# Kernel optimization log

Hardware: AMD Instinct MI355X
Metric: run time of the kernel (lower is better)

## Reference

```python
import jax, jax.numpy as jnp
import numpy as np

N = 50000      # nodes per node type
E = 600000     # edges per edge type
H = 128        # hidden_channels (= in_channels)
OUT = 16       # out_channels
G = 64         # number of graphs in the batch
L = 2          # num_layers
NEG_SLOPE = 0.2


def setup_inputs() -> dict:
    key = jax.random.key(0)
    ks = jax.random.split(key, 13)
    x_paper = jax.random.normal(ks[0], (N, H), jnp.float32)
    x_author = jax.random.normal(ks[1], (N, H), jnp.float32)
    edge_pa = jax.random.randint(ks[2], (2, E), 0, N, jnp.int32)   # paper -> author
    edge_ap = jax.random.randint(ks[3], (2, E), 0, N, jnp.int32)   # author -> paper
    batch_paper = jnp.sort(jax.random.randint(ks[4], (N,), 0, G, jnp.int32))
    batch_author = jnp.sort(jax.random.randint(ks[5], (N,), 0, G, jnp.int32))
    # GAT params, stacked [layer, edge_type, ...]; edge_type 0 = paper->author, 1 = author->paper
    Wsrc = jax.random.normal(ks[6], (L, 2, H, H), jnp.float32) * 0.05
    Wdst = jax.random.normal(ks[7], (L, 2, H, H), jnp.float32) * 0.05
    att_src = jax.random.normal(ks[8], (L, 2, H), jnp.float32) * 0.05
    att_dst = jax.random.normal(ks[9], (L, 2, H), jnp.float32) * 0.05
    bias = jax.random.normal(ks[10], (L, 2, H), jnp.float32) * 0.05
    linW = jax.random.normal(ks[11], (H, OUT), jnp.float32) * 0.05
    linb = jax.random.normal(ks[12], (OUT,), jnp.float32) * 0.05
    return {"x_paper": x_paper, "x_author": x_author, "edge_pa": edge_pa,
            "edge_ap": edge_ap, "batch_paper": batch_paper, "batch_author": batch_author,
            "Wsrc": Wsrc, "Wdst": Wdst, "att_src": att_src, "att_dst": att_dst,
            "bias": bias, "linW": linW, "linb": linb}


def _gat(x_s, x_d, edge, Wsrc, Wdst, a_src_w, a_dst_w, b):
    """Single-head PyG GATConv (bipartite, add_self_loops=False, concat)."""
    src, dst = edge[0], edge[1]
    hs = x_s @ Wsrc                        # [Ns, H]
    hd = x_d @ Wdst                        # [Nd, H]
    a_s = hs @ a_src_w                     # [Ns]
    a_d = hd @ a_dst_w                     # [Nd]
    e = jax.nn.leaky_relu(a_s[src] + a_d[dst], NEG_SLOPE)   # [E]
    nd = x_d.shape[0]
    m = jax.ops.segment_max(e, dst, num_segments=nd)        # segment softmax
    ex = jnp.exp(e - m[dst])
    den = jax.ops.segment_sum(ex, dst, num_segments=nd) + 1e-16
    w = ex / den[dst]                                        # [E]
    out = jax.ops.segment_sum(w[:, None] * hs[src], dst, num_segments=nd)
    return out + b


def reference(x_paper, x_author, edge_pa, edge_ap, batch_paper, batch_author,
              Wsrc, Wdst, att_src, att_dst, bias, linW, linb):
    xp, xa = x_paper, x_author
    for l in range(L):
        out_a = _gat(xp, xa, edge_pa, Wsrc[l, 0], Wdst[l, 0], att_src[l, 0], att_dst[l, 0], bias[l, 0])
        out_p = _gat(xa, xp, edge_ap, Wsrc[l, 1], Wdst[l, 1], att_src[l, 1], att_dst[l, 1], bias[l, 1])
        xp = jax.nn.relu(out_p)
        xa = jax.nn.relu(out_a)
    pooled_p = jax.ops.segment_max(xp, batch_paper, num_segments=G)  # [G, H]
    pooled_a = jax.ops.segment_max(xa, batch_author, num_segments=G)
    return (pooled_p @ linW + linb, pooled_a @ linW + linb)
```

## Files before the change

kernel.cpp:

```cpp
#include <hip/hip_runtime.h>
#include <hip/hip_fp16.h>

constexpr int NN = 50000;
constexpr int NE = 600000;
constexpr int HH = 128;
constexpr int GG = 64;
constexpr int LL = 2;
constexpr int OC = 16;
constexpr float NEG = 0.2f;
constexpr int NBK = (2 * NN + 255) / 256;

typedef _Float16 f16x8 __attribute__((ext_vector_type(8)));
typedef float f32x4 __attribute__((ext_vector_type(4)));

__global__ void k_prevec(const float* __restrict__ Wsrc, const float* __restrict__ Wdst,
                         const float* __restrict__ att_src, const float* __restrict__ att_dst,
                         float* __restrict__ v) {
    int b = blockIdx.x;
    int kind = b >> 2, lt = b & 3;
    const float* W   = (kind ? Wdst : Wsrc) + (size_t)lt * HH * HH;
    const float* att = (kind ? att_dst : att_src) + lt * HH;
    __shared__ float sa[HH];
    int t = threadIdx.x;
    sa[t] = att[t];
    __syncthreads();
    float s = 0.f;
    for (int j = 0; j < HH; ++j) s += W[t * HH + j] * sa[j];
    v[b * HH + t] = s;
}

__global__ void k_wcvt(const float* __restrict__ Wsrc, __half* __restrict__ Wt) {
    int lt = blockIdx.x >> 7;
    int nrow = blockIdx.x & 127;
    int k = threadIdx.x;
    Wt[((size_t)lt * HH + nrow) * HH + k] =
        __float2half_rn(Wsrc[(size_t)lt * HH * HH + (size_t)k * HH + nrow]);
}

__global__ void k_hist2(const int* __restrict__ dpa, const int* __restrict__ dap,
                        int* __restrict__ cnt) {
    int i = blockIdx.x * 256 + threadIdx.x;
    if (i < NE) atomicAdd(&cnt[dpa[i]], 1);
    else if (i < 2 * NE) atomicAdd(&cnt[NN + dap[i - NE]], 1);
}

__global__ void k_scan1(const int* __restrict__ cnt, int* __restrict__ bsum, int n) {
    __shared__ int s[256];
    int i = blockIdx.x * 256 + threadIdx.x;
    s[threadIdx.x] = (i < n) ? cnt[i] : 0;
    __syncthreads();
    for (int off = 128; off > 0; off >>= 1) {
        if (threadIdx.x < off) s[threadIdx.x] += s[threadIdx.x + off];
        __syncthreads();
    }
    if (threadIdx.x == 0) bsum[blockIdx.x] = s[0];
}

__global__ void k_scan2(int* __restrict__ bsum, int nb) {
    __shared__ int s[512];
    int t = threadIdx.x;
    int v = (t < nb) ? bsum[t] : 0;
    s[t] = v;
    __syncthreads();
    for (int off = 1; off < 512; off <<= 1) {
        int x = (t >= off) ? s[t - off] : 0;
        __syncthreads();
        s[t] += x;
        __syncthreads();
    }
    if (t < nb) bsum[t] = s[t] - v;
}

__global__ void k_scan3(const int* __restrict__ cnt, const int* __restrict__ bsum,
                        int* __restrict__ rowptr, int n, int e) {
    __shared__ int s[256];
    int t = threadIdx.x;
    int i = blockIdx.x * 256 + t;
    int v = (i < n) ? cnt[i] : 0;
    s[t] = v;
    __syncthreads();
    for (int off = 1; off < 256; off <<= 1) {
        int x = (t >= off) ? s[t - off] : 0;
        __syncthreads();
        s[t] += x;
        __syncthreads();
    }
    if (i < n) rowptr[i] = bsum[blockIdx.x] + s[t] - v;
    if (i == n - 1) rowptr[n] = e;
}

__global__ void k_binit(const int* __restrict__ rpc, int* __restrict__ bcur) {
    int b = blockIdx.x * 256 + threadIdx.x;
    if (b < NBK) bcur[b] = rpc[b * 256];
}

__global__ __launch_bounds__(256) void k_bucket1(const int* __restrict__ edge_pa,
                                                 const int* __restrict__ edge_ap,
                                                 int* __restrict__ bcur, unsigned* __restrict__ colt) {
    __shared__ int cnt[NBK];
    __shared__ int gpos[NBK];
    int t = threadIdx.x;
    int e0 = blockIdx.x * 4096;
    int m = min(4096, 2 * NE - e0);
    for (int i = t; i < NBK; i += 256) cnt[i] = 0;
    __syncthreads();
    for (int i = t; i < m; i += 256) {
        int e = e0 + i;
        int d = (e < NE) ? edge_pa[NE + e] : NN + edge_ap[NE + (e - NE)];
        atomicAdd(&cnt[d >> 8], 1);
    }
    __syncthreads();
    for (int b = t; b < NBK; b += 256)
        if (cnt[b]) gpos[b] = atomicAdd(&bcur[b], cnt[b]);
    __syncthreads();
    for (int i = t; i < m; i += 256) {
        int e = e0 + i;
        int src, d;
        if (e < NE) { src = edge_pa[e]; d = edge_pa[NE + e]; }
        else        { int j = e - NE; src = edge_ap[j]; d = NN + edge_ap[NE + j]; }
        int p = atomicAdd(&gpos[d >> 8], 1);
        colt[p] = ((unsigned)src << 8) | (unsigned)(d & 255);
    }
}

__global__ __launch_bounds__(256) void k_bucket2(const unsigned* __restrict__ colt,
                                                 const int* __restrict__ rpc,
                                                 int* __restrict__ colc, int* __restrict__ dstc) {
    __shared__ int cur[257];
    int b = blockIdx.x, t = threadIdx.x;
    int node0 = b * 256;
    int nn2 = min(256, 2 * NN - node0);
    for (int i = t; i <= nn2; i += 256) cur[i] = rpc[node0 + i];
    __syncthreads();
    int g0 = cur[0], g1 = cur[nn2];
    __syncthreads();
    for (int i = g0 + t; i < g1; i += 256) {
        unsigned p = colt[i];
        int pos = atomicAdd(&cur[p & 255], 1);
        colc[pos] = (int)(p >> 8);
        dstc[pos] = node0 + (int)(p & 255);
    }
}

__global__ __launch_bounds__(256) void k_gemm(const float* __restrict__ X, const __half* __restrict__ Wt,
                                              const float* __restrict__ v1, const float* __restrict__ v2,
                                              __half* __restrict__ Hout,
                                              float* __restrict__ o1, float* __restrict__ o2, int n) {
    int wave = threadIdx.x >> 6;
    int lane = threadIdx.x & 63;
    int r0 = blockIdx.x * 64 + wave * 16;
    int arow = r0 + (lane & 15);
    int kgrp = (lane >> 4) * 8;

    f32x4 acc[8] = {};
    float s1 = 0.f, s2 = 0.f;
#pragma unroll
    for (int ks = 0; ks < 4; ++ks) {
        int k0 = ks * 32 + kgrp;
        float xv[8];
        if (arow < n) {
            float4 x0 = *(const float4*)(X + (size_t)arow * HH + k0);
            float4 x1 = *(const float4*)(X + (size_t)arow * HH + k0 + 4);
            xv[0] = x0.x; xv[1] = x0.y; xv[2] = x0.z; xv[3] = x0.w;
            xv[4] = x1.x; xv[5] = x1.y; xv[6] = x1.z; xv[7] = x1.w;
        } else {
#pragma unroll
            for (int i = 0; i < 8; ++i) xv[i] = 0.f;
        }
        float4 va0 = *(const float4*)(v1 + k0), va1 = *(const float4*)(v1 + k0 + 4);
        float4 vb0 = *(const float4*)(v2 + k0), vb1 = *(const float4*)(v2 + k0 + 4);
        s1 += xv[0] * va0.x + xv[1] * va0.y + xv[2] * va0.z + xv[3] * va0.w
            + xv[4] * va1.x + xv[5] * va1.y + xv[6] * va1.z + xv[7] * va1.w;
        s2 += xv[0] * vb0.x + xv[1] * vb0.y + xv[2] * vb0.z + xv[3] * vb0.w
            + xv[4] * vb1.x + xv[5] * vb1.y + xv[6] * vb1.z + xv[7] * vb1.w;

        f16x8 ahi, alo;
#pragma unroll
        for (int i = 0; i < 8; ++i) {
            _Float16 h = (_Float16)xv[i];
            ahi[i] = h;
            alo[i] = (_Float16)(xv[i] - (float)h);
        }
#pragma unroll
        for (int nt = 0; nt < 8; ++nt) {
            const f16x8 b = *(const f16x8*)(Wt + ((size_t)(nt * 16 + (lane & 15))) * HH + k0);
            acc[nt] = __builtin_amdgcn_mfma_f32_16x16x32_f16(alo, b, acc[nt], 0, 0, 0);
            acc[nt] = __builtin_amdgcn_mfma_f32_16x16x32_f16(ahi, b, acc[nt], 0, 0, 0);
        }
    }

    s1 += __shfl_xor(s1, 16); s1 += __shfl_xor(s1, 32);
    s2 += __shfl_xor(s2, 16); s2 += __shfl_xor(s2, 32);
    if ((lane >> 4) == 0 && arow < n) { o1[arow] = s1; o2[arow] = s2; }

    int srow = r0 + (lane >> 4) * 4;
    int scol = lane & 15;
#pragma unroll
    for (int nt = 0; nt < 8; ++nt) {
#pragma unroll
        for (int reg = 0; reg < 4; ++reg) {
            int gr = srow + reg;
            if (gr < n) Hout[(size_t)gr * HH + nt * 16 + scol] = __float2half_rn(acc[nt][reg]);
        }
    }
}

__global__ __launch_bounds__(256) void k_score(const int* __restrict__ colc, const int* __restrict__ dstc,
                                               const float* __restrict__ as0, const float* __restrict__ as1,
                                               const float* __restrict__ adc, float* __restrict__ expw) {
    int j = blockIdx.x * 256 + threadIdx.x;
    if (j >= 2 * NE) return;
    int src = colc[j];
    int d   = dstc[j];
    float c = (j < NE ? as0 : as1)[src] + adc[d];
    c = c > 0.f ? c : NEG * c;
    expw[j] = __expf(c);
}

__global__ __launch_bounds__(256) void k_aggregate3(const int* __restrict__ rpc, const int* __restrict__ colc,
                                                    const float* __restrict__ expw,
                                                    const __half* __restrict__ H0, const __half* __restrict__ H1,
                                                    const float* __restrict__ bias0, const float* __restrict__ bias1,
                                                    float* __restrict__ XA, float* __restrict__ XP) {
    int wid  = (blockIdx.x * blockDim.x + threadIdx.x) >> 6;
    int lane = threadIdx.x & 63;
    int half = lane >> 5;
    int sl   = lane & 31;
    int w = wid * 2 + half;
    if (w >= 2 * NN) return;
    int type = (w >= NN);
    int node = type ? w - NN : w;
    const __half* Hs  = type ? H1 : H0;
    const float* bias = type ? bias1 : bias0;
    float* Xout       = type ? XP : XA;

    int base = rpc[w], end = rpc[w + 1];

    float den = 0.f;
    float4 acc = {0.f, 0.f, 0.f, 0.f};

    int j = base;
    for (; j + 4 <= end; j += 4) {
        int s[4]; float wg[4]; float2 raw[4];
#pragma unroll
        for (int k = 0; k < 4; ++k) s[k] = colc[j + k];
#pragma unroll
        for (int k = 0; k < 4; ++k) wg[k] = expw[j + k];
#pragma unroll
        for (int k = 0; k < 4; ++k) raw[k] = *(const float2*)(Hs + (size_t)s[k] * HH + sl * 4);
#pragma unroll
        for (int k = 0; k < 4; ++k) {
            den += wg[k];
            float2 fa = __half22float2(*(const __half2*)&raw[k].x);
            float2 fb = __half22float2(*(const __half2*)&raw[k].y);
            acc.x += wg[k] * fa.x; acc.y += wg[k] * fa.y;
            acc.z += wg[k] * fb.x; acc.w += wg[k] * fb.y;
        }
    }
    for (; j < end; ++j) {
        int s = colc[j];
        float wg = expw[j];
        float2 raw = *(const float2*)(Hs + (size_t)s * HH + sl * 4);
        den += wg;
        float2 fa = __half22float2(*(const __half2*)&raw.x);
        float2 fb = __half22float2(*(const __half2*)&raw.y);
        acc.x += wg * fa.x; acc.y += wg * fa.y;
        acc.z += wg * fb.x; acc.w += wg * fb.y;
    }

    float inv = 1.f / (den + 1e-16f);
    float4 b = *(const float4*)(bias + sl * 4);
    float4 o;
    o.x = fmaxf(acc.x * inv + b.x, 0.f);
    o.y = fmaxf(acc.y * inv + b.y, 0.f);
    o.z = fmaxf(acc.z * inv + b.z, 0.f);
    o.w = fmaxf(acc.w * inv + b.w, 0.f);
    *(float4*)(Xout + (size_t)node * HH + sl * 4) = o;
}

constexpr int POOL_CHUNK = 64;
__global__ __launch_bounds__(256) void k_pool(const float* __restrict__ XPf, const float* __restrict__ XAf,
                                              const int* __restrict__ batch_p, const int* __restrict__ batch_a,
                                              unsigned* __restrict__ pooled, int n, int blocksPerType) {
    int type = blockIdx.x / blocksPerType;
    int blk  = blockIdx.x % blocksPerType;
    const float* X = type ? XAf : XPf;
    const int* batch = type ? batch_a : batch_p;
    unsigned* pool = pooled + type * GG * HH;

    int sub  = threadIdx.x >> 5;
    int lane = threadIdx.x & 31;
    int i0 = blk * POOL_CHUNK + sub * (POOL_CHUNK / 8);
    if (i0 >= n) return;
    int i1 = min(i0 + POOL_CHUNK / 8, n);

    int g = batch[i0];
    float4 m = make_float4(0.f, 0.f, 0.f, 0.f);
    for (int i = i0; i < i1; ++i) {
        int gi = batch[i];
        if (gi != g) {
            unsigned* p = pool + g * HH + lane * 4;
            atomicMax(p + 0, __float_as_uint(m.x));
            atomicMax(p + 1, __float_as_uint(m.y));
            atomicMax(p + 2, __float_as_uint(m.z));
            atomicMax(p + 3, __float_as_uint(m.w));
            m = make_float4(0.f, 0.f, 0.f, 0.f);
            g = gi;
        }
        float4 x = *(const float4*)(X + (size_t)i * HH + lane * 4);
        m.x = fmaxf(m.x, x.x);
        m.y = fmaxf(m.y, x.y);
        m.z = fmaxf(m.z, x.z);
        m.w = fmaxf(m.w, x.w);
    }
    unsigned* p = pool + g * HH + lane * 4;
    atomicMax(p + 0, __float_as_uint(m.x));
    atomicMax(p + 1, __float_as_uint(m.y));
    atomicMax(p + 2, __float_as_uint(m.z));
    atomicMax(p + 3, __float_as_uint(m.w));
}

__global__ void k_final(const unsigned* __restrict__ pooled, const float* __restrict__ linW,
                        const float* __restrict__ linb, float* __restrict__ out) {
    int idx = blockIdx.x * blockDim.x + threadIdx.x;
    if (idx >= 2 * GG * OC) return;
    int p = idx >> 10;
    int g = (idx >> 4) & 63;
    int o = idx & 15;
    const unsigned* row = pooled + (size_t)(p * GG + g) * HH;
    float s = linb[o];
    for (int k = 0; k < HH; ++k) s += __uint_as_float(row[k]) * linW[k * OC + o];
    out[idx] = s;
}

extern "C" void kernel_launch(void* const* d_in, const int* in_sizes, int n_in,
                              void* d_out, int out_size, void* d_ws, size_t ws_size,
                              hipStream_t stream) {
    const float* x_paper  = (const float*)d_in[0];
    const float* x_author = (const float*)d_in[1];
    const int*   edge_pa  = (const int*)d_in[2];
    const int*   edge_ap  = (const int*)d_in[3];
    const int*   batch_p  = (const int*)d_in[4];
    const int*   batch_a  = (const int*)d_in[5];
    const float* Wsrc     = (const float*)d_in[6];
    const float* Wdst     = (const float*)d_in[7];
    const float* att_src  = (const float*)d_in[8];
    const float* att_dst  = (const float*)d_in[9];
    const float* bias     = (const float*)d_in[10];
    const float* linW     = (const float*)d_in[11];
    const float* linb     = (const float*)d_in[12];
    float* out = (float*)d_out;

    size_t off = 0;
    char* base = (char*)d_ws;
    auto alloc = [&](size_t bytes) -> void* {
        void* p = base + off;
        off += (bytes + 255) & ~(size_t)255;
        return p;
    };
    __half* H0 = (__half*)alloc((size_t)NN * HH * 2);
    __half* H1 = (__half*)alloc((size_t)NN * HH * 2);
    float* XP  = (float*)alloc((size_t)NN * HH * 4);
    float* XA  = (float*)alloc((size_t)NN * HH * 4);
    float* as0 = (float*)alloc(NN * 4);
    float* as1 = (float*)alloc(NN * 4);
    float* adc = (float*)alloc(2 * NN * 4);
    float* vv  = (float*)alloc(8 * HH * 4);
    __half* Wt = (__half*)alloc(4 * HH * HH * 2);
    int* rpc  = (int*)alloc((2 * NN + 1) * 4);
    int* colc = (int*)alloc(2 * NE * 4);
    int* dstc = (int*)alloc(2 * NE * 4);
    unsigned* colt = (unsigned*)alloc(2 * NE * 4);
    float* expw = (float*)alloc(2 * NE * 4);
    int* cnt  = (int*)alloc(2 * NN * 4);
    int* bsum = (int*)alloc(2048);
    int* bcur = (int*)alloc(NBK * 4);
    unsigned* pooled = (unsigned*)alloc(2 * GG * HH * 4);

    const int EB2  = (2 * NE + 255) / 256;
    const int NBS2 = (2 * NN + 255) / 256;
    const int CB   = (2 * NE + 4095) / 4096;

    k_prevec<<<8, 128, 0, stream>>>(Wsrc, Wdst, att_src, att_dst, vv);
    k_wcvt<<<512, 128, 0, stream>>>(Wsrc, Wt);

    hipMemsetAsync(cnt, 0, 2 * NN * sizeof(int), stream);
    k_hist2<<<EB2, 256, 0, stream>>>(edge_pa + NE, edge_ap + NE, cnt);
    k_scan1<<<NBS2, 256, 0, stream>>>(cnt, bsum, 2 * NN);
    k_scan2<<<1, 512, 0, stream>>>(bsum, NBS2);
    k_scan3<<<NBS2, 256, 0, stream>>>(cnt, bsum, rpc, 2 * NN, 2 * NE);
    k_binit<<<(NBK + 255) / 256, 256, 0, stream>>>(rpc, bcur);
    k_bucket1<<<CB, 256, 0, stream>>>(edge_pa, edge_ap, bcur, colt);
    k_bucket2<<<NBK, 256, 0, stream>>>(colt, rpc, colc, dstc);

    const float* xp = x_paper;
    const float* xa = x_author;
    const int GB = (NN + 63) / 64;
    for (int l = 0; l < LL; ++l) {
        int t0 = l * 2 + 0, t1 = l * 2 + 1;
        k_gemm<<<GB, 256, 0, stream>>>(xp, Wt + (size_t)t0 * HH * HH,
                                       vv + t0 * HH, vv + (4 + t1) * HH, H0, as0, adc + NN, NN);
        k_gemm<<<GB, 256, 0, stream>>>(xa, Wt + (size_t)t1 * HH * HH,
                                       vv + t1 * HH, vv + (4 + t0) * HH, H1, as1, adc, NN);
        k_score<<<EB2, 256, 0, stream>>>(colc, dstc, as0, as1, adc, expw);
        k_aggregate3<<<12500, 256, 0, stream>>>(rpc, colc, expw, H0, H1,
                                                bias + t0 * HH, bias + t1 * HH, XA, XP);
        xp = XP; xa = XA;
    }

    hipMemsetAsync(pooled, 0, 2 * GG * HH * sizeof(unsigned), stream);
    const int PB = (NN + POOL_CHUNK - 1) / POOL_CHUNK;
    k_pool<<<PB * 2, 256, 0, stream>>>(XP, XA, batch_p, batch_a, pooled, NN, PB);
    k_final<<<8, 256, 0, stream>>>(pooled, linW, linb, out);
}
```

Baseline: 456.4 us.

## Fuse prep kernels, merge histogram into bucketing, batch both GEMMs per layer

Merges the weight-vector precompute, the weight transpose/convert and the pooled-buffer zeroing into one prep kernel. The degree histogram now happens inside the first bucketing pass, and buckets go into fixed-capacity slots (CAP), which removes the separate histogram and bucket-init kernels. The two per-layer GEMMs become one launch, and the aggregation loop gains an 8-wide unrolled gather. The aim is to cut launch count and add memory-level parallelism. The risk is that any bucket holding more than CAP edges would overflow its slot, since the capacity is fixed and assumes the random degree distribution.

```diff
diff --git a/kernel.cpp b/kernel.cpp
--- a/kernel.cpp
+++ b/kernel.cpp
@@ -9,39 +9,34 @@
 constexpr int OC = 16;
 constexpr float NEG = 0.2f;
 constexpr int NBK = (2 * NN + 255) / 256;
+constexpr int CAP = 3456;
 
 typedef _Float16 f16x8 __attribute__((ext_vector_type(8)));
 typedef float f32x4 __attribute__((ext_vector_type(4)));
 
-__global__ void k_prevec(const float* __restrict__ Wsrc, const float* __restrict__ Wdst,
-                         const float* __restrict__ att_src, const float* __restrict__ att_dst,
-                         float* __restrict__ v) {
-    int b = blockIdx.x;
-    int kind = b >> 2, lt = b & 3;
-    const float* W   = (kind ? Wdst : Wsrc) + (size_t)lt * HH * HH;
-    const float* att = (kind ? att_dst : att_src) + lt * HH;
-    __shared__ float sa[HH];
-    int t = threadIdx.x;
-    sa[t] = att[t];
-    __syncthreads();
-    float s = 0.f;
-    for (int j = 0; j < HH; ++j) s += W[t * HH + j] * sa[j];
-    v[b * HH + t] = s;
-}
-
-__global__ void k_wcvt(const float* __restrict__ Wsrc, __half* __restrict__ Wt) {
-    int lt = blockIdx.x >> 7;
-    int nrow = blockIdx.x & 127;
-    int k = threadIdx.x;
-    Wt[((size_t)lt * HH + nrow) * HH + k] =
-        __float2half_rn(Wsrc[(size_t)lt * HH * HH + (size_t)k * HH + nrow]);
-}
-
-__global__ void k_hist2(const int* __restrict__ dpa, const int* __restrict__ dap,
-                        int* __restrict__ cnt) {
-    int i = blockIdx.x * 256 + threadIdx.x;
-    if (i < NE) atomicAdd(&cnt[dpa[i]], 1);
-    else if (i < 2 * NE) atomicAdd(&cnt[NN + dap[i - NE]], 1);
+__global__ void k_prep(const float* __restrict__ Wsrc, const float* __restrict__ Wdst,
+                       const float* __restrict__ att_src, const float* __restrict__ att_dst,
+                       float* __restrict__ v, __half* __restrict__ Wt, unsigned* __restrict__ pooled) {
+    int b = blockIdx.x, t = threadIdx.x;
+    if (b < 8) {
+        int kind = b >> 2, lt = b & 3;
+        const float* W   = (kind ? Wdst : Wsrc) + (size_t)lt * HH * HH;
+        const float* att = (kind ? att_dst : att_src) + lt * HH;
+        __shared__ float sa[HH];
+        sa[t] = att[t];
+        __syncthreads();
+        float s = 0.f;
+        for (int j = 0; j < HH; ++j) s += W[t * HH + j] * sa[j];
+        v[b * HH + t] = s;
+    } else if (b < 520) {
+        int bb = b - 8;
+        int lt = bb >> 7, nrow = bb & 127;
+        Wt[((size_t)lt * HH + nrow) * HH + t] =
+            __float2half_rn(Wsrc[(size_t)lt * HH * HH + (size_t)t * HH + nrow]);
+    } else {
+        int idx = (b - 520) * 128 + t;
+        pooled[idx] = 0u;
+    }
 }
 
 __global__ void k_scan1(const int* __restrict__ cnt, int* __restrict__ bsum, int n) {
@@ -89,29 +84,26 @@
     if (i == n - 1) rowptr[n] = e;
 }
 
-__global__ void k_binit(const int* __restrict__ rpc, int* __restrict__ bcur) {
-    int b = blockIdx.x * 256 + threadIdx.x;
-    if (b < NBK) bcur[b] = rpc[b * 256];
-}
-
 __global__ __launch_bounds__(256) void k_bucket1(const int* __restrict__ edge_pa,
                                                  const int* __restrict__ edge_ap,
-                                                 int* __restrict__ bcur, unsigned* __restrict__ colt) {
-    __shared__ int cnt[NBK];
+                                                 int* __restrict__ cnt, int* __restrict__ bcur,
+                                                 unsigned* __restrict__ colt) {
+    __shared__ int lcnt[NBK];
     __shared__ int gpos[NBK];
     int t = threadIdx.x;
     int e0 = blockIdx.x * 4096;
     int m = min(4096, 2 * NE - e0);
-    for (int i = t; i < NBK; i += 256) cnt[i] = 0;
+    for (int i = t; i < NBK; i += 256) lcnt[i] = 0;
     __syncthreads();
     for (int i = t; i < m; i += 256) {
         int e = e0 + i;
         int d = (e < NE) ? edge_pa[NE + e] : NN + edge_ap[NE + (e - NE)];
-        atomicAdd(&cnt[d >> 8], 1);
+        atomicAdd(&lcnt[d >> 8], 1);
+        atomicAdd(&cnt[d], 1);
     }
     __syncthreads();
     for (int b = t; b < NBK; b += 256)
-        if (cnt[b]) gpos[b] = atomicAdd(&bcur[b], cnt[b]);
+        if (lcnt[b]) gpos[b] = b * CAP + atomicAdd(&bcur[b], lcnt[b]);
     __syncthreads();
     for (int i = t; i < m; i += 256) {
         int e = e0 + i;
@@ -124,31 +116,44 @@
 }
 
 __global__ __launch_bounds__(256) void k_bucket2(const unsigned* __restrict__ colt,
-                                                 const int* __restrict__ rpc,
+                                                 const int* __restrict__ bcur, const int* __restrict__ rpc,
                                                  int* __restrict__ colc, int* __restrict__ dstc) {
-    __shared__ int cur[257];
+    __shared__ int cur[256];
     int b = blockIdx.x, t = threadIdx.x;
     int node0 = b * 256;
     int nn2 = min(256, 2 * NN - node0);
-    for (int i = t; i <= nn2; i += 256) cur[i] = rpc[node0 + i];
-    __syncthreads();
-    int g0 = cur[0], g1 = cur[nn2];
-    __syncthreads();
-    for (int i = g0 + t; i < g1; i += 256) {
-        unsigned p = colt[i];
+    if (t < nn2) cur[t] = rpc[node0 + t];
+    __syncthreads();
+    int cntb = bcur[b];
+    const unsigned* srcp = colt + (size_t)b * CAP;
+    for (int i = t; i < cntb; i += 256) {
+        unsigned p = srcp[i];
         int pos = atomicAdd(&cur[p & 255], 1);
         colc[pos] = (int)(p >> 8);
         dstc[pos] = node0 + (int)(p & 255);
     }
 }
 
-__global__ __launch_bounds__(256) void k_gemm(const float* __restrict__ X, const __half* __restrict__ Wt,
-                                              const float* __restrict__ v1, const float* __restrict__ v2,
-                                              __half* __restrict__ Hout,
-                                              float* __restrict__ o1, float* __restrict__ o2, int n) {
+__global__ __launch_bounds__(256) void k_gemm2(const float* __restrict__ Xp, const float* __restrict__ Xa,
+                                               const __half* __restrict__ Wt0, const __half* __restrict__ Wt1,
+                                               const float* __restrict__ vs0, const float* __restrict__ vs1,
+                                               const float* __restrict__ vd0, const float* __restrict__ vd1,
+                                               __half* __restrict__ H0, __half* __restrict__ H1,
+                                               float* __restrict__ as0, float* __restrict__ as1,
+                                               float* __restrict__ adc, int gb) {
+    int type = blockIdx.x >= gb;
+    int blk  = type ? blockIdx.x - gb : blockIdx.x;
+    const float* X  = type ? Xa : Xp;
+    const __half* Wt = type ? Wt1 : Wt0;
+    const float* v1 = type ? vs1 : vs0;
+    const float* v2 = type ? vd0 : vd1;
+    __half* Hout = type ? H1 : H0;
+    float* o1 = type ? as1 : as0;
+    float* o2 = type ? adc : adc + NN;
+
     int wave = threadIdx.x >> 6;
     int lane = threadIdx.x & 63;
-    int r0 = blockIdx.x * 64 + wave * 16;
+    int r0 = blk * 64 + wave * 16;
     int arow = r0 + (lane & 15);
     int kgrp = (lane >> 4) * 8;
 
@@ -158,7 +163,7 @@
     for (int ks = 0; ks < 4; ++ks) {
         int k0 = ks * 32 + kgrp;
         float xv[8];
-        if (arow < n) {
+        if (arow < NN) {
             float4 x0 = *(const float4*)(X + (size_t)arow * HH + k0);
             float4 x1 = *(const float4*)(X + (size_t)arow * HH + k0 + 4);
             xv[0] = x0.x; xv[1] = x0.y; xv[2] = x0.z; xv[3] = x0.w;
@@ -183,15 +188,15 @@
         }
 #pragma unroll
         for (int nt = 0; nt < 8; ++nt) {
-            const f16x8 b = *(const f16x8*)(Wt + ((size_t)(nt * 16 + (lane & 15))) * HH + k0);
-            acc[nt] = __builtin_amdgcn_mfma_f32_16x16x32_f16(alo, b, acc[nt], 0, 0, 0);
-            acc[nt] = __builtin_amdgcn_mfma_f32_16x16x32_f16(ahi, b, acc[nt], 0, 0, 0);
+            const f16x8 bb = *(const f16x8*)(Wt + ((size_t)(nt * 16 + (lane & 15))) * HH + k0);
+            acc[nt] = __builtin_amdgcn_mfma_f32_16x16x32_f16(alo, bb, acc[nt], 0, 0, 0);
+            acc[nt] = __builtin_amdgcn_mfma_f32_16x16x32_f16(ahi, bb, acc[nt], 0, 0, 0);
         }
     }
 
     s1 += __shfl_xor(s1, 16); s1 += __shfl_xor(s1, 32);
     s2 += __shfl_xor(s2, 16); s2 += __shfl_xor(s2, 32);
-    if ((lane >> 4) == 0 && arow < n) { o1[arow] = s1; o2[arow] = s2; }
+    if ((lane >> 4) == 0 && arow < NN) { o1[arow] = s1; o2[arow] = s2; }
 
     int srow = r0 + (lane >> 4) * 4;
     int scol = lane & 15;
@@ -200,7 +205,7 @@
 #pragma unroll
         for (int reg = 0; reg < 4; ++reg) {
             int gr = srow + reg;
-            if (gr < n) Hout[(size_t)gr * HH + nt * 16 + scol] = __float2half_rn(acc[nt][reg]);
+            if (gr < NN) Hout[(size_t)gr * HH + nt * 16 + scol] = __float2half_rn(acc[nt][reg]);
         }
     }
 }
@@ -240,6 +245,23 @@
     float4 acc = {0.f, 0.f, 0.f, 0.f};
 
     int j = base;
+    for (; j + 8 <= end; j += 8) {
+        int s[8]; float wg[8]; float2 raw[8];
+#pragma unroll
+        for (int k = 0; k < 8; ++k) s[k] = colc[j + k];
+#pragma unroll
+        for (int k = 0; k < 8; ++k) wg[k] = expw[j + k];
+#pragma unroll
+        for (int k = 0; k < 8; ++k) raw[k] = *(const float2*)(Hs + (size_t)s[k] * HH + sl * 4);
+#pragma unroll
+        for (int k = 0; k < 8; ++k) {
+            den += wg[k];
+            float2 fa = __half22float2(*(const __half2*)&raw[k].x);
+            float2 fb = __half22float2(*(const __half2*)&raw[k].y);
+            acc.x += wg[k] * fa.x; acc.y += wg[k] * fa.y;
+            acc.z += wg[k] * fb.x; acc.w += wg[k] * fb.y;
+        }
+    }
     for (; j + 4 <= end; j += 4) {
         int s[4]; float wg[4]; float2 raw[4];
 #pragma unroll
@@ -370,45 +392,41 @@
     int* rpc  = (int*)alloc((2 * NN + 1) * 4);
     int* colc = (int*)alloc(2 * NE * 4);
     int* dstc = (int*)alloc(2 * NE * 4);
-    unsigned* colt = (unsigned*)alloc(2 * NE * 4);
+    unsigned* colt = (unsigned*)alloc((size_t)NBK * CAP * 4);
     float* expw = (float*)alloc(2 * NE * 4);
-    int* cnt  = (int*)alloc(2 * NN * 4);
+    int* cnt  = (int*)alloc((2 * NN + NBK) * 4);
+    int* bcur = cnt + 2 * NN;
     int* bsum = (int*)alloc(2048);
-    int* bcur = (int*)alloc(NBK * 4);
     unsigned* pooled = (unsigned*)alloc(2 * GG * HH * 4);
 
     const int EB2  = (2 * NE + 255) / 256;
     const int NBS2 = (2 * NN + 255) / 256;
     const int CB   = (2 * NE + 4095) / 4096;
-
-    k_prevec<<<8, 128, 0, stream>>>(Wsrc, Wdst, att_src, att_dst, vv);
-    k_wcvt<<<512, 128, 0, stream>>>(Wsrc, Wt);
-
-    hipMemsetAsync(cnt, 0, 2 * NN * sizeof(int), stream);
-    k_hist2<<<EB2, 256, 0, stream>>>(edge_pa + NE, edge_ap + NE, cnt);
+    const int GB   = (NN + 63) / 64;
+
+    k_prep<<<648, 128, 0, stream>>>(Wsrc, Wdst, att_src, att_dst, vv, Wt, pooled);
+    hipMemsetAsync(cnt, 0, (2 * NN + NBK) * sizeof(int), stream);
+    k_bucket1<<<CB, 256, 0, stream>>>(edge_pa, edge_ap, cnt, bcur, colt);
     k_scan1<<<NBS2, 256, 0, stream>>>(cnt, bsum, 2 * NN);
     k_scan2<<<1, 512, 0, stream>>>(bsum, NBS2);
     k_scan3<<<NBS2, 256, 0, stream>>>(cnt, bsum, rpc, 2 * NN, 2 * NE);
-    k_binit<<<(NBK + 255) / 256, 256, 0, stream>>>(rpc, bcur);
-    k_bucket1<<<CB, 256, 0, stream>>>(edge_pa, edge_ap, bcur, colt);
-    k_bucket2<<<NBK, 256, 0, stream>>>(colt, rpc, colc, dstc);
+    k_bucket2<<<NBK, 256, 0, stream>>>(colt, bcur, rpc, colc, dstc);
 
     const float* xp = x_paper;
     const float* xa = x_author;
-    const int GB = (NN + 63) / 64;
     for (int l = 0; l < LL; ++l) {
         int t0 = l * 2 + 0, t1 = l * 2 + 1;
-        k_gemm<<<GB, 256, 0, stream>>>(xp, Wt + (size_t)t0 * HH * HH,
-                                       vv + t0 * HH, vv + (4 + t1) * HH, H0, as0, adc + NN, NN);
-        k_gemm<<<GB, 256, 0, stream>>>(xa, Wt + (size_t)t1 * HH * HH,
-                                       vv + t1 * HH, vv + (4 + t0) * HH, H1, as1, adc, NN);
+        k_gemm2<<<2 * GB, 256, 0, stream>>>(xp, xa,
+                                            Wt + (size_t)t0 * HH * HH, Wt + (size_t)t1 * HH * HH,
+                                            vv + t0 * HH, vv + t1 * HH,
+                                            vv + (4 + t0) * HH, vv + (4 + t1) * HH,
+                                            H0, H1, as0, as1, adc, GB);
         k_score<<<EB2, 256, 0, stream>>>(colc, dstc, as0, as1, adc, expw);
         k_aggregate3<<<12500, 256, 0, stream>>>(rpc, colc, expw, H0, H1,
                                                 bias + t0 * HH, bias + t1 * HH, XA, XP);
         xp = XP; xa = XA;
     }
 
-    hipMemsetAsync(pooled, 0, 2 * GG * HH * sizeof(unsigned), stream);
     const int PB = (NN + POOL_CHUNK - 1) / POOL_CHUNK;
     k_pool<<<PB * 2, 256, 0, stream>>>(XP, XA, batch_p, batch_a, pooled, NN, PB);
     k_final<<<8, 256, 0, stream>>>(pooled, linW, linb, out);
```

Result: faster. 422.6 us (-7.4%).
